# Optimization experiments

Hardware: AMD Instinct MI355X
Metric: run time of the kernel (lower is better)

## Reference

```python
import jax, jax.numpy as jnp
import numpy as np

NF = 64            # n_filter
CFAC = 3           # SinSobel c_factor: identity + sobel-x + sobel-y
FIN = NF * CFAC    # dyna block input channels (192)
FH = NF * 2        # dyna hidden (128)
FOUT = NF          # dyna output (64)
LAT = 512
N_CALLS = 6        # ceil(log2(128) - log2(2))
P_SIZES = [FH * FIN, FH, FH * FH, FH, FOUT * FH, FOUT, FOUT * FIN, FOUT]
P_TOTAL = sum(P_SIZES)  # 61824
_OFFS = np.cumsum([0] + P_SIZES)

def act(t):
    return jax.nn.leaky_relu(t, 0.2)

def conv1x1(x, w, b):
    # x [B,I,H,W], w [O,I] -> [B,O,H,W]
    return jnp.einsum('bihw,oi->bohw', x, w) + b[None, :, None, None]

def res_block(x, w0, b0, w1, b1):
    # GAN-stability style residual block with 1x1 convs
    return x + 0.1 * conv1x1(act(conv1x1(act(x), w0, b0)), w1, b1)

def depthwise3x3(x, k2d):
    C = x.shape[1]
    k = jnp.broadcast_to(k2d.astype(x.dtype), (C, 1, 3, 3))
    return jax.lax.conv_general_dilated(
        x, k, (1, 1), [(1, 1), (1, 1)],
        dimension_numbers=('NCHW', 'OIHW', 'NCHW'),
        feature_group_count=C)

SOBEL_X = jnp.array([[1., 0., -1.], [2., 0., -2.], [1., 0., -1.]], jnp.float32) / 8.0
SOBEL_Y = SOBEL_X.T
_g = jnp.exp(-0.5 * jnp.array([-1., 0., 1.], jnp.float32) ** 2)
GAUSS = jnp.outer(_g, _g)
GAUSS = GAUSS / GAUSS.sum()

def sin_sobel(x):
    return jnp.concatenate([x, depthwise3x3(x, SOBEL_X), depthwise3x3(x, SOBEL_Y)], axis=1)

def dyna_residual(x, params):
    # per-sample hypernetwork-generated 1x1-conv residual block
    B = x.shape[0]
    def take(i, shape):
        return params[:, _OFFS[i]:_OFFS[i + 1]].reshape((B,) + shape)
    w_in, b_in = take(0, (FH, FIN)), take(1, (FH,))
    w_mid, b_mid = take(2, (FH, FH)), take(3, (FH,))
    w_out, b_out = take(4, (FOUT, FH)), take(5, (FOUT,))
    w_sk, b_sk = take(6, (FOUT, FIN)), take(7, (FOUT,))
    def pconv(h, w, b):  # batched per-sample 1x1 conv
        return jnp.einsum('bihw,boi->bohw', h, w) + b[:, :, None, None]
    x_s = pconv(x, w_sk, b_sk)
    dx = pconv(x, w_in, b_in)
    dx = pconv(act(dx), w_mid, b_mid)
    dx = pconv(act(dx), w_out, b_out)
    return x_s + dx

def downsample(x):
    # GaussianSmoothing(k=3, sigma=1, pad=1) then bilinear 0.5
    # (align_corners=False bilinear at scale 0.5 == 2x2 average pooling)
    x = depthwise3x3(x, GAUSS)
    B, C, H, W = x.shape
    return x.reshape(B, C, H // 2, 2, W // 2, 2).mean(axis=(3, 5))

def lin_res(x, w1, b1, w2, b2, sw=None, sb=None):
    x_s = x if sw is None else x @ sw + sb
    return x_s + 0.1 * (act(act(x) @ w1 + b1) @ w2 + b2)

def forward(x, inj_lat, leak, in_w, in_b, inrb_w0, inrb_b0, inrb_w1, inrb_b1,
            hyp_w, hyp_b, outrb_w0, outrb_b0, outrb_w1, outrb_b1,
            l1_sw, l1_sb, l1_w1, l1_b1, l1_w2, l1_b2,
            l2_w1, l2_b1, l2_w2, l2_b2, lo_w, lo_b):
    out = conv1x1(x, in_w, in_b)
    out = res_block(out, inrb_w0, inrb_b0, inrb_w1, inrb_b1)
    leak_f = jnp.clip(leak, 0.001, 1000.0)
    dyn_params = inj_lat @ hyp_w + hyp_b  # [B, P_TOTAL], shared across calls
    out_embs = [out]
    for _ in range(N_CALLS):  # fixed small layer loop; spatial dims halve each call
        out_new = sin_sobel(out)
        out_new = dyna_residual(out_new, dyn_params)
        out = out + leak_f * out_new
        out = downsample(out)
        out_embs.append(out)
    out = res_block(out, outrb_w0, outrb_b0, outrb_w1, outrb_b1)
    h = out.mean(axis=(2, 3))  # [B, NF]
    h = lin_res(h, l1_w1, l1_b1, l1_w2, l1_b2, l1_sw, l1_sb)
    h = lin_res(h, l2_w1, l2_b1, l2_w2, l2_b2)
    lat = h @ lo_w + lo_b
    return lat, out_embs

def setup_inputs() -> dict:
    key = jax.random.key(0)
    ks = jax.random.split(key, 24)
    B, C, S = 8, 3, 128
    def rn(k, shape, scale=0.05):
        return scale * jax.random.normal(k, shape, jnp.float32)
    z = lambda n: jnp.zeros((n,), jnp.float32)
    return {
        'x': jax.random.normal(ks[0], (B, C, S, S), jnp.float32),
        'inj_lat': jax.random.normal(ks[1], (B, LAT), jnp.float32),
        'leak': jnp.array(0.1, jnp.float32),
        'in_w': rn(ks[2], (NF, C)), 'in_b': z(NF),
        'inrb_w0': rn(ks[3], (NF, NF)), 'inrb_b0': z(NF),
        'inrb_w1': rn(ks[4], (NF, NF)), 'inrb_b1': z(NF),
        'hyp_w': rn(ks[5], (LAT, P_TOTAL), 0.01), 'hyp_b': rn(ks[6], (P_TOTAL,), 0.01),
        'outrb_w0': rn(ks[7], (NF, NF)), 'outrb_b0': z(NF),
        'outrb_w1': rn(ks[8], (NF, NF)), 'outrb_b1': z(NF),
        'l1_sw': rn(ks[9], (NF, LAT)), 'l1_sb': z(LAT),
        'l1_w1': rn(ks[10], (NF, 2 * LAT)), 'l1_b1': z(2 * LAT),
        'l1_w2': rn(ks[11], (2 * LAT, LAT)), 'l1_b2': z(LAT),
        'l2_w1': rn(ks[12], (LAT, LAT)), 'l2_b1': z(LAT),
        'l2_w2': rn(ks[13], (LAT, LAT)), 'l2_b2': z(LAT),
        'lo_w': rn(ks[14], (LAT, LAT)), 'lo_b': z(LAT),
    }

def reference(x, inj_lat, leak, in_w, in_b, inrb_w0, inrb_b0, inrb_w1, inrb_b1,
              hyp_w, hyp_b, outrb_w0, outrb_b0, outrb_w1, outrb_b1,
              l1_sw, l1_sb, l1_w1, l1_b1, l1_w2, l1_b2,
              l2_w1, l2_b1, l2_w2, l2_b2, lo_w, lo_b):
    lat, out_embs = forward(x, inj_lat, leak, in_w, in_b, inrb_w0, inrb_b0, inrb_w1, inrb_b1,
                            hyp_w, hyp_b, outrb_w0, outrb_b0, outrb_w1, outrb_b1,
                            l1_sw, l1_sb, l1_w1, l1_b1, l1_w2, l1_b2,
                            l2_w1, l2_b1, l2_w2, l2_b2, lo_w, lo_b)
    return (lat, *out_embs)
```

## Files before the change

### kernel.cpp

```cpp
#include <hip/hip_runtime.h>


#define BATCH 8
#define PT 61824

typedef __attribute__((ext_vector_type(8))) short bf16x8;
typedef __attribute__((ext_vector_type(4))) float f32x4;

__device__ __forceinline__ float lrelu(float v) { return v > 0.f ? v : 0.2f * v; }

__device__ __forceinline__ short f2bf(float f) {
    union { float fv; unsigned u; } v; v.fv = f;
    return (short)((v.u + 0x7fffu + ((v.u >> 16) & 1u)) >> 16);
}

__device__ __forceinline__ unsigned cvt_pk_bf16(float lo, float hi) {
    unsigned r;
    asm("v_cvt_pk_bf16_f32 %0, %1, %2" : "=v"(r) : "v"(lo), "v"(hi));
    return r;
}
__device__ __forceinline__ short f2bf1(float f) {
    unsigned r;
    asm("v_cvt_pk_bf16_f32 %0, %1, %1" : "=v"(r) : "v"(f));
    return (short)r;
}

__global__ __launch_bounds__(256) void hyper_kernel(
    const float* __restrict__ inj, const float* __restrict__ hw,
    const float* __restrict__ hb, float* __restrict__ dyn,
    short* __restrict__ dyn16)
{
    __shared__ float s_l[512 * 8];
    __shared__ float s_part[3 * 8 * 64];
    int t = threadIdx.x;
    for (int i = t; i < 4096; i += 256) {
        int b = i >> 9, k = i & 511;
        s_l[k * 8 + b] = inj[i];
    }
    __syncthreads();
    int po = t & 63, kq = t >> 6;
    int p = blockIdx.x * 64 + po;
    float acc[8];
#pragma unroll
    for (int b = 0; b < 8; ++b) acc[b] = 0.f;
    for (int k = kq * 128; k < kq * 128 + 128; ++k) {
        float w = hw[(size_t)k * PT + p];
        float4 a0 = *(const float4*)&s_l[k * 8];
        float4 a1 = *(const float4*)&s_l[k * 8 + 4];
        acc[0] += a0.x * w; acc[1] += a0.y * w; acc[2] += a0.z * w; acc[3] += a0.w * w;
        acc[4] += a1.x * w; acc[5] += a1.y * w; acc[6] += a1.z * w; acc[7] += a1.w * w;
    }
    if (kq > 0) {
#pragma unroll
        for (int b = 0; b < 8; ++b) s_part[((kq - 1) * 8 + b) * 64 + po] = acc[b];
    }
    __syncthreads();
    if (kq == 0) {
        float bias = hb[p];
        bool isb = (p >= 24576 && p < 24704) || (p >= 41088 && p < 41216)
                || (p >= 49408 && p < 49472) || (p >= 61760);
#pragma unroll
        for (int b = 0; b < 8; ++b) {
            float v = acc[b] + s_part[b * 64 + po] + s_part[(8 + b) * 64 + po]
                    + s_part[(16 + b) * 64 + po] + bias;
            if (isb) dyn[(size_t)b * PT + p] = v;
            dyn16[(size_t)b * PT + p] = f2bf1(v);
        }
    }
}

__global__ __launch_bounds__(256) void stem_kernel(
    const float* __restrict__ x, const float* __restrict__ in_w,
    const float* __restrict__ in_b,
    const float* __restrict__ w0, const float* __restrict__ b0,
    const float* __restrict__ w1, const float* __restrict__ b1,
    float* __restrict__ out0)
{
    const int HW = 128 * 128;
    __shared__ float s_t0[64 * 68];
    __shared__ short s_vh[2 * 64 * 72];
    __shared__ float s_x[192];
    short* s_v = s_vh;
    short* s_h = s_vh + 64 * 72;
    float* s_y = (float*)s_vh;

    const int b = blockIdx.x >> 8;
    const int tile = blockIdx.x & 255;
    const int pix0 = tile * 64;
    const int t = threadIdx.x;
    const int l = t & 63, w = t >> 6;
    const int lp = l & 15, lq = l >> 4;

    if (t < 192) s_x[t] = x[(size_t)b * 3 * HW + (t >> 6) * HW + pix0 + (t & 63)];
    __syncthreads();

    for (int j = t; j < 1024; j += 256) {
        int p = j & 63, cg = j >> 6;
        float x0 = s_x[p], x1 = s_x[64 + p], x2 = s_x[128 + p];
        short pk[4];
#pragma unroll
        for (int cc = 0; cc < 4; ++cc) {
            int c = cg * 4 + cc;
            float v = in_b[c] + x0 * in_w[c * 3] + x1 * in_w[c * 3 + 1]
                    + x2 * in_w[c * 3 + 2];
            s_t0[c * 68 + p] = v;
            pk[cc] = f2bf1(lrelu(v));
        }
        *(short4*)&s_v[p * 72 + cg * 4] = make_short4(pk[0], pk[1], pk[2], pk[3]);
    }
    __syncthreads();

    const int o = w * 16 + lp;
    const f32x4 z4 = {0.f, 0.f, 0.f, 0.f};

    bf16x8 wb0[2], wb1[2];
#pragma unroll
    for (int k = 0; k < 2; ++k) {
        bf16x8 p0, p1;
#pragma unroll
        for (int e = 0; e < 8; ++e) {
            p0[e] = f2bf1(w0[o * 64 + k * 32 + lq * 8 + e]);
            p1[e] = f2bf1(w1[o * 64 + k * 32 + lq * 8 + e]);
        }
        wb0[k] = p0; wb1[k] = p1;
    }

    {
        float bi = b0[o];
        f32x4 acc[4];
#pragma unroll
        for (int mt = 0; mt < 4; ++mt) acc[mt] = z4;
#pragma unroll
        for (int k = 0; k < 2; ++k)
#pragma unroll
            for (int mt = 0; mt < 4; ++mt) {
                bf16x8 a = *(const bf16x8*)&s_v[(mt * 16 + lp) * 72 + k * 32 + lq * 8];
                acc[mt] = __builtin_amdgcn_mfma_f32_16x16x32_bf16(a, wb0[k], acc[mt], 0, 0, 0);
            }
#pragma unroll
        for (int mt = 0; mt < 4; ++mt)
#pragma unroll
            for (int r = 0; r < 4; ++r)
                s_h[(mt * 16 + lq * 4 + r) * 72 + o] = f2bf1(lrelu(acc[mt][r] + bi));
    }
    __syncthreads();

    {
        float bi = b1[o];
        f32x4 acc[4];
#pragma unroll
        for (int mt = 0; mt < 4; ++mt) acc[mt] = z4;
#pragma unroll
        for (int k = 0; k < 2; ++k)
#pragma unroll
            for (int mt = 0; mt < 4; ++mt) {
                bf16x8 a = *(const bf16x8*)&s_h[(mt * 16 + lp) * 72 + k * 32 + lq * 8];
                acc[mt] = __builtin_amdgcn_mfma_f32_16x16x32_bf16(a, wb1[k], acc[mt], 0, 0, 0);
            }
        __syncthreads();
#pragma unroll
        for (int mt = 0; mt < 4; ++mt) {
            f32x4 dv;
#pragma unroll
            for (int r = 0; r < 4; ++r) dv[r] = 0.1f * (acc[mt][r] + bi);
            *(f32x4*)&s_y[o * 68 + mt * 16 + lq * 4] = dv;
        }
    }
    __syncthreads();

#pragma unroll
    for (int v = 0; v < 4; ++v) {
        int idx = v * 1024 + t * 4;
        int oo = idx >> 6, px = idx & 63;
        f32x4 t0v = *(const f32x4*)&s_t0[oo * 68 + px];
        f32x4 dv = *(const f32x4*)&s_y[oo * 68 + px];
        f32x4 ov = t0v + dv;
        *(f32x4*)&out0[((size_t)b * 64 + oo) * HW + pix0 + px] = ov;
    }
}

template<int MT>
__global__ __launch_bounds__(256, 4) void iter_kernel(
    const float* __restrict__ cur, const float* __restrict__ dynf,
    const short* __restrict__ dynb, const float* __restrict__ leak_p,
    float* __restrict__ y, int S, int sh)
{
    constexpr int PX = MT * 16;
    constexpr int SY = (MT == 4) ? 68 : 20;
    __shared__ short s_s[PX * 192];
    __shared__ short s_h[PX * 128];
    float* s_y = (float*)s_s;

    const int HW = S * S;
    const int tilesPer = HW / PX;
    const int nwg = BATCH * tilesPer;
    const int rb = (int)blockIdx.x;
    const int lb = (rb & 7) * (nwg >> 3) + (rb >> 3);
    const int b = lb / tilesPer;
    const int tile = lb - b * tilesPer;
    const int pix0 = tile * PX;
    const int t = threadIdx.x;
    const int l = t & 63, w = t >> 6;
    const int lp = l & 15, lq = l >> 4;
    const float* base = cur + (size_t)b * 64 * HW;
    const float lk = fminf(fmaxf(leak_p[0], 0.001f), 1000.f);

    {
        const int p = (MT == 4) ? (lp + 16 * w) : lp;
        const int rxw = (p & 7) << 2;
        const int gpx = pix0 + p;
        const int row = gpx >> sh;
        const int x = gpx & (S - 1);
        const bool rm = (row > 0), rp = (row < S - 1);
        const bool le = (lp == 0) && (x > 0);
        const bool re = (lp == 15) && (x < S - 1);
        constexpr int iters = (MT == 4) ? 8 : 2;
        int* s32 = (int*)s_s;
#pragma unroll
        for (int i = 0; i < iters; ++i) {
            const int cp = (MT == 4) ? (lq + 4 * i) : (lq + 4 * w + 16 * i);
            float v0s[2], sxs[2], sys[2];
#pragma unroll
            for (int cc = 0; cc < 2; ++cc) {
                const int c = 2 * cp + cc;
                const float* ch = base + (size_t)c * HW + row * S;
                float vm = rm ? ch[x - S] : 0.f;
                float v0 = ch[x];
                float vp = rp ? ch[x + S] : 0.f;
                float elm = 0.f, el0 = 0.f, elp = 0.f, erm = 0.f, er0 = 0.f, erp = 0.f;
                if (le) { elm = rm ? ch[x - 1 - S] : 0.f; el0 = ch[x - 1]; elp = rp ? ch[x - 1 + S] : 0.f; }
                if (re) { erm = rm ? ch[x + 1 - S] : 0.f; er0 = ch[x + 1]; erp = rp ? ch[x + 1 + S] : 0.f; }
                float Lm = __shfl(vm, l - 1), L0 = __shfl(v0, l - 1), Lp = __shfl(vp, l - 1);
                float Rm = __shfl(vm, l + 1), R0 = __shfl(v0, l + 1), Rp = __shfl(vp, l + 1);
                if (lp == 0)  { Lm = elm; L0 = el0; Lp = elp; }
                if (lp == 15) { Rm = erm; R0 = er0; Rp = erp; }
                if (x == 0)     { Lm = 0.f; L0 = 0.f; Lp = 0.f; }
                if (x == S - 1) { Rm = 0.f; R0 = 0.f; Rp = 0.f; }
                v0s[cc] = v0;
                sxs[cc] = (Lm - Rm + 2.f * (L0 - R0) + Lp - Rp) * 0.125f;
                sys[cc] = (Lm + 2.f * vm + Rm - Lp - 2.f * vp - Rp) * 0.125f;
            }
            const int cpx_ = cp ^ rxw;
            s32[p * 96 + cpx_] = (int)cvt_pk_bf16(v0s[0], v0s[1]);
            s32[p * 96 + 32 + cpx_] = (int)cvt_pk_bf16(sxs[0], sxs[1]);
            s32[p * 96 + 64 + cpx_] = (int)cvt_pk_bf16(sys[0], sys[1]);
        }
    }
    __syncthreads();

    const short* wb = dynb + (size_t)b * PT;
    const float* pf = dynf + (size_t)b * PT;
    const f32x4 z4 = {0.f, 0.f, 0.f, 0.f};
    const int sx4 = (lp & 7) << 4;
    const char* ss_b = (const char*)s_s;
    const char* sh_cb = (const char*)s_h;
    char* sh_b = (char*)s_h;

    f32x4 acc_sk[MT];
#pragma unroll
    for (int mt = 0; mt < MT; ++mt) acc_sk[mt] = z4;

    {
        const float bi0 = pf[24576 + (w * 2) * 16 + lp];
        const float bi1 = pf[24576 + (w * 2 + 1) * 16 + lp];
        f32x4 acc[2][MT];
#pragma unroll
        for (int n = 0; n < 2; ++n)
#pragma unroll
            for (int mt = 0; mt < MT; ++mt) acc[n][mt] = z4;
        const int osk = w * 16 + lp;
#pragma unroll 2
        for (int k = 0; k < 6; ++k) {
            bf16x8 a[MT];
#pragma unroll
            for (int mt = 0; mt < MT; ++mt)
                a[mt] = *(const bf16x8*)(ss_b + (mt * 16 + lp) * 384 + ((k * 64 + lq * 16) ^ sx4));
#pragma unroll
            for (int n = 0; n < 2; ++n) {
                int o = (w * 2 + n) * 16 + lp;
                bf16x8 bb = *(const bf16x8*)&wb[o * 192 + k * 32 + lq * 8];
#pragma unroll
                for (int mt = 0; mt < MT; ++mt)
                    acc[n][mt] = __builtin_amdgcn_mfma_f32_16x16x32_bf16(a[mt], bb, acc[n][mt], 0, 0, 0);
            }
            {
                bf16x8 bsk = *(const bf16x8*)&wb[49472 + osk * 192 + k * 32 + lq * 8];
#pragma unroll
                for (int mt = 0; mt < MT; ++mt)
                    acc_sk[mt] = __builtin_amdgcn_mfma_f32_16x16x32_bf16(a[mt], bsk, acc_sk[mt], 0, 0, 0);
            }
        }
#pragma unroll
        for (int n = 0; n < 2; ++n) {
            int o = (w * 2 + n) * 16 + lp;
            float bi = n ? bi1 : bi0;
#pragma unroll
            for (int mt = 0; mt < MT; ++mt)
#pragma unroll
                for (int r = 0; r < 4; ++r) {
                    int row = mt * 16 + lq * 4 + r;
                    *(short*)(sh_b + row * 256 + ((o * 2) ^ ((row & 7) << 4))) =
                        f2bf1(lrelu(acc[n][mt][r] + bi));
                }
        }
    }
    __syncthreads();

    {
        const float bi0 = pf[41088 + (w * 2) * 16 + lp];
        const float bi1 = pf[41088 + (w * 2 + 1) * 16 + lp];
        f32x4 acc[2][MT];
#pragma unroll
        for (int n = 0; n < 2; ++n)
#pragma unroll
            for (int mt = 0; mt < MT; ++mt) acc[n][mt] = z4;
#pragma unroll 2
        for (int k = 0; k < 4; ++k) {
            bf16x8 a[MT];
#pragma unroll
            for (int mt = 0; mt < MT; ++mt)
                a[mt] = *(const bf16x8*)(sh_cb + (mt * 16 + lp) * 256 + ((k * 64 + lq * 16) ^ sx4));
#pragma unroll
            for (int n = 0; n < 2; ++n) {
                int o = (w * 2 + n) * 16 + lp;
                bf16x8 bb = *(const bf16x8*)&wb[24704 + o * 128 + k * 32 + lq * 8];
#pragma unroll
                for (int mt = 0; mt < MT; ++mt)
                    acc[n][mt] = __builtin_amdgcn_mfma_f32_16x16x32_bf16(a[mt], bb, acc[n][mt], 0, 0, 0);
            }
        }
        __syncthreads();
#pragma unroll
        for (int n = 0; n < 2; ++n) {
            int o = (w * 2 + n) * 16 + lp;
            float bi = n ? bi1 : bi0;
#pragma unroll
            for (int mt = 0; mt < MT; ++mt)
#pragma unroll
                for (int r = 0; r < 4; ++r) {
                    int row = mt * 16 + lq * 4 + r;
                    *(short*)(sh_b + row * 256 + ((o * 2) ^ ((row & 7) << 4))) =
                        f2bf1(lrelu(acc[n][mt][r] + bi));
                }
        }
    }
    __syncthreads();

    {
        int o = w * 16 + lp;
        const float bi = pf[49408 + o] + pf[61760 + o];
        f32x4 acc[MT];
#pragma unroll
        for (int mt = 0; mt < MT; ++mt) acc[mt] = acc_sk[mt];
#pragma unroll 2
        for (int k = 0; k < 4; ++k) {
            bf16x8 bb = *(const bf16x8*)&wb[41216 + o * 128 + k * 32 + lq * 8];
#pragma unroll
            for (int mt = 0; mt < MT; ++mt) {
                bf16x8 a = *(const bf16x8*)(sh_cb + (mt * 16 + lp) * 256 + ((k * 64 + lq * 16) ^ sx4));
                acc[mt] = __builtin_amdgcn_mfma_f32_16x16x32_bf16(a, bb, acc[mt], 0, 0, 0);
            }
        }
#pragma unroll
        for (int mt = 0; mt < MT; ++mt) {
            f32x4 dv;
#pragma unroll
            for (int r = 0; r < 4; ++r) dv[r] = acc[mt][r] + bi;
            *(f32x4*)&s_y[o * SY + mt * 16 + lq * 4] = dv;
        }
    }
    __syncthreads();

    {
        if (MT == 4) {
#pragma unroll
            for (int v = 0; v < 4; ++v) {
                int idx = v * 1024 + t * 4;
                int o = idx >> 6, px = idx & 63;
                f32x4 sv = *(const f32x4*)&s_y[o * SY + px];
                const float* cb = cur + ((size_t)b * 64 + o) * HW + pix0 + px;
                float* yb = y + ((size_t)b * 64 + o) * HW + pix0 + px;
                f32x4 cv = *(const f32x4*)cb;
                *(f32x4*)yb = cv + lk * sv;
            }
        } else {
            int o = t >> 2, px = (t & 3) * 4;
            f32x4 sv = *(const f32x4*)&s_y[o * SY + px];
            const float* cb = cur + ((size_t)b * 64 + o) * HW + pix0 + px;
            float* yb = y + ((size_t)b * 64 + o) * HW + pix0 + px;
            f32x4 cv = *(const f32x4*)cb;
            *(f32x4*)yb = cv + lk * sv;
        }
    }
}

__global__ __launch_bounds__(256) void down_kernel(
    const float* __restrict__ yin, float* __restrict__ outp,
    int S, int S2, int TW, int CPB, int tiles)
{
    __shared__ float s_in[3072];
    __shared__ float s_hb[1152];

    const float ga = 0.60653065971263342f;
    const float gs = 1.f / ((1.f + 2.f * ga) * (1.f + 2.f * ga));
    const float u0 = ga, u1 = 1.f + ga;

    const int t = threadIdx.x;
    const int nwg = (int)gridDim.x;
    const int rb = (int)blockIdx.x;
    const int bi = (rb & 7) * (nwg >> 3) + (rb >> 3);
    const int tix = bi % tiles;
    const int rem = bi / tiles;
    const int tiy = rem % tiles;
    const int cg = rem / tiles;
    const int bc0 = cg * CPB;

    const int IH = 2 * TW + 2;
    const int IW = IH;
    const int IWP = IW + 2;
    const int HS = TW + 1;
    const int gy0 = tiy * 2 * TW - 1;
    const int gx0 = tix * 2 * TW - 1;

    const int loadTot = CPB * IH * IW;
    for (int j = t; j < loadTot; j += 256) {
        int c = j / (IH * IW);
        int r = j - c * (IH * IW);
        int iy = r / IW, ix = r - iy * IW;
        int gy = gy0 + iy, gx = gx0 + ix;
        float v = 0.f;
        if (gy >= 0 && gy < S && gx >= 0 && gx < S)
            v = yin[(size_t)(bc0 + c) * S * S + gy * S + gx];
        s_in[(c * IH + iy) * IWP + ix] = v;
    }
    __syncthreads();

    const int hTot = CPB * IH * TW;
    for (int j = t; j < hTot; j += 256) {
        int c = j / (IH * TW);
        int r = j - c * (IH * TW);
        int iy = r / TW, ox = r - iy * TW;
        const float* pin = &s_in[(c * IH + iy) * IWP + 2 * ox];
        s_hb[(c * IH + iy) * HS + ox] =
            u0 * (pin[0] + pin[3]) + u1 * (pin[1] + pin[2]);
    }
    __syncthreads();

    {
        int ox = t % TW;
        int r = t / TW;
        int oy = r % TW;
        int c = r / TW;
        const float* ph = &s_hb[(c * IH + 2 * oy) * HS + ox];
        float acc = u0 * (ph[0] + ph[3 * HS]) + u1 * (ph[HS] + ph[2 * HS]);
        outp[(size_t)(bc0 + c) * S2 * S2 + (tiy * TW + oy) * S2 + tix * TW + ox] =
            acc * 0.25f * gs;
    }
}

__global__ __launch_bounds__(256) void head_a_kernel(
    const float* __restrict__ emb6,
    const float* __restrict__ w0, const float* __restrict__ b0,
    const float* __restrict__ w1, const float* __restrict__ b1,
    float* __restrict__ h)
{
    __shared__ float sm_t[256], sm_v[256], sm_r[256];
    int b = blockIdx.x, t = threadIdx.x;
    sm_t[t] = emb6[b * 256 + t];
    __syncthreads();
    {
        int o = t & 63, p = t >> 6;
        float acc = 0.f;
        for (int k = 0; k < 64; ++k) acc += w0[o * 64 + k] * lrelu(sm_t[k * 4 + p]);
        sm_v[o * 4 + p] = lrelu(acc + b0[o]);
    }
    __syncthreads();
    {
        int o = t & 63, p = t >> 6;
        float acc = 0.f;
        for (int k = 0; k < 64; ++k) acc += w1[o * 64 + k] * sm_v[k * 4 + p];
        sm_r[o * 4 + p] = sm_t[o * 4 + p] + 0.1f * (acc + b1[o]);
    }
    __syncthreads();
    if (t < 64)
        h[b * 64 + t] = 0.25f * (sm_r[t * 4] + sm_r[t * 4 + 1] + sm_r[t * 4 + 2] + sm_r[t * 4 + 3]);
}

__global__ __launch_bounds__(256) void head_b_kernel(
    const float* __restrict__ h, const float* __restrict__ w,
    const float* __restrict__ bias, float* __restrict__ t1)
{
    __shared__ float s_h[64];
    int id = blockIdx.x * 256 + threadIdx.x;
    int b = id >> 10, o = id & 1023;
    if (threadIdx.x < 64) s_h[threadIdx.x] = lrelu(h[b * 64 + threadIdx.x]);
    __syncthreads();
    float acc = 0.f;
    for (int k = 0; k < 64; ++k) acc += s_h[k] * w[k * 1024 + o];
    t1[b * 1024 + o] = lrelu(acc + bias[o]);
}

__global__ __launch_bounds__(256) void head_c_kernel(
    const float* __restrict__ h, const float* __restrict__ t1,
    const float* __restrict__ sw, const float* __restrict__ sb,
    const float* __restrict__ w2, const float* __restrict__ b2,
    float* __restrict__ h1)
{
    __shared__ float s_t[8 * 128];
    __shared__ float s_h[8 * 64];
    int oblk = blockIdx.x & 1, chunk = blockIdx.x >> 1;
    int t = threadIdx.x;
    int o = oblk * 256 + t;
    for (int j = t; j < 1024; j += 256) {
        int b = j >> 7, kk = j & 127;
        s_t[j] = t1[b * 1024 + chunk * 128 + kk];
    }
    if (chunk == 0)
        for (int j = t; j < 512; j += 256) s_h[j] = h[j];
    __syncthreads();
    float acc[8];
#pragma unroll
    for (int b = 0; b < 8; ++b) acc[b] = 0.f;
    for (int kk = 0; kk < 128; ++kk) {
        float wv = w2[(chunk * 128 + kk) * 512 + o];
#pragma unroll
        for (int b = 0; b < 8; ++b) acc[b] += s_t[b * 128 + kk] * wv;
    }
#pragma unroll
    for (int b = 0; b < 8; ++b) acc[b] *= 0.1f;
    if (chunk == 0) {
        for (int k = 0; k < 64; ++k) {
            float wv = sw[k * 512 + o];
#pragma unroll
            for (int b = 0; b < 8; ++b) acc[b] += s_h[b * 64 + k] * wv;
        }
        float c0 = sb[o] + 0.1f * b2[o];
#pragma unroll
        for (int b = 0; b < 8; ++b) acc[b] += c0;
    }
#pragma unroll
    for (int b = 0; b < 8; ++b) atomicAdd(&h1[b * 512 + o], acc[b]);
}

__global__ __launch_bounds__(256) void head_d_kernel(
    const float* __restrict__ h1, const float* __restrict__ w,
    const float* __restrict__ bias, float* __restrict__ z3)
{
    __shared__ float s_u[8 * 64];
    int oblk = blockIdx.x & 1, chunk = blockIdx.x >> 1;
    int t = threadIdx.x;
    int o = oblk * 256 + t;
    for (int j = t; j < 512; j += 256) {
        int b = j >> 6, kk = j & 63;
        s_u[j] = lrelu(h1[b * 512 + chunk * 64 + kk]);
    }
    __syncthreads();
    float acc[8];
#pragma unroll
    for (int b = 0; b < 8; ++b) acc[b] = 0.f;
    for (int kk = 0; kk < 64; ++kk) {
        float wv = w[(chunk * 64 + kk) * 512 + o];
#pragma unroll
        for (int b = 0; b < 8; ++b) acc[b] += s_u[b * 64 + kk] * wv;
    }
    if (chunk == 0) {
        float c0 = bias[o];
#pragma unroll
        for (int b = 0; b < 8; ++b) acc[b] += c0;
    }
#pragma unroll
    for (int b = 0; b < 8; ++b) atomicAdd(&z3[b * 512 + o], acc[b]);
}

__global__ __launch_bounds__(256) void head_e_kernel(
    const float* __restrict__ h1, const float* __restrict__ z3,
    const float* __restrict__ w, const float* __restrict__ bias,
    float* __restrict__ h2)
{
    __shared__ float s_u[8 * 64];
    int oblk = blockIdx.x & 1, chunk = blockIdx.x >> 1;
    int t = threadIdx.x;
    int o = oblk * 256 + t;
    for (int j = t; j < 512; j += 256) {
        int b = j >> 6, kk = j & 63;
        s_u[j] = lrelu(z3[b * 512 + chunk * 64 + kk]);
    }
    __syncthreads();
    float acc[8];
#pragma unroll
    for (int b = 0; b < 8; ++b) acc[b] = 0.f;
    for (int kk = 0; kk < 64; ++kk) {
        float wv = w[(chunk * 64 + kk) * 512 + o];
#pragma unroll
        for (int b = 0; b < 8; ++b) acc[b] += s_u[b * 64 + kk] * wv;
    }
#pragma unroll
    for (int b = 0; b < 8; ++b) acc[b] *= 0.1f;
    if (chunk == 0) {
        float c0 = 0.1f * bias[o];
#pragma unroll
        for (int b = 0; b < 8; ++b) acc[b] += h1[b * 512 + o] + c0;
    }
#pragma unroll
    for (int b = 0; b < 8; ++b) atomicAdd(&h2[b * 512 + o], acc[b]);
}

__global__ __launch_bounds__(256) void head_f_kernel(
    const float* __restrict__ h2, const float* __restrict__ w,
    const float* __restrict__ bias, float* __restrict__ lat)
{
    __shared__ float s_u[8 * 64];
    int oblk = blockIdx.x & 1, chunk = blockIdx.x >> 1;
    int t = threadIdx.x;
    int o = oblk * 256 + t;
    for (int j = t; j < 512; j += 256) {
        int b = j >> 6, kk = j & 63;
        s_u[j] = h2[b * 512 + chunk * 64 + kk];
    }
    __syncthreads();
    float acc[8];
#pragma unroll
    for (int b = 0; b < 8; ++b) acc[b] = 0.f;
    for (int kk = 0; kk < 64; ++kk) {
        float wv = w[(chunk * 64 + kk) * 512 + o];
#pragma unroll
        for (int b = 0; b < 8; ++b) acc[b] += s_u[b * 64 + kk] * wv;
    }
    if (chunk == 0) {
        float c0 = bias[o];
#pragma unroll
        for (int b = 0; b < 8; ++b) acc[b] += c0;
    }
#pragma unroll
    for (int b = 0; b < 8; ++b) atomicAdd(&lat[b * 512 + o], acc[b]);
}

extern "C" void kernel_launch(void* const* d_in, const int* in_sizes, int n_in,
                              void* d_out, int out_size, void* d_ws, size_t ws_size,
                              hipStream_t stream) {
    const float* x      = (const float*)d_in[0];
    const float* inj    = (const float*)d_in[1];
    const float* leak   = (const float*)d_in[2];
    const float* in_w   = (const float*)d_in[3];
    const float* in_b   = (const float*)d_in[4];
    const float* inrb_w0 = (const float*)d_in[5];
    const float* inrb_b0 = (const float*)d_in[6];
    const float* inrb_w1 = (const float*)d_in[7];
    const float* inrb_b1 = (const float*)d_in[8];
    const float* hyp_w  = (const float*)d_in[9];
    const float* hyp_b  = (const float*)d_in[10];
    const float* outrb_w0 = (const float*)d_in[11];
    const float* outrb_b0 = (const float*)d_in[12];
    const float* outrb_w1 = (const float*)d_in[13];
    const float* outrb_b1 = (const float*)d_in[14];
    const float* l1_sw  = (const float*)d_in[15];
    const float* l1_sb  = (const float*)d_in[16];
    const float* l1_w1  = (const float*)d_in[17];
    const float* l1_b1  = (const float*)d_in[18];
    const float* l1_w2  = (const float*)d_in[19];
    const float* l1_b2  = (const float*)d_in[20];
    const float* l2_w1  = (const float*)d_in[21];
    const float* l2_b1  = (const float*)d_in[22];
    const float* l2_w2  = (const float*)d_in[23];
    const float* l2_b2  = (const float*)d_in[24];
    const float* lo_w   = (const float*)d_in[25];
    const float* lo_b   = (const float*)d_in[26];

    float* out = (float*)d_out;
    float* dyn = (float*)d_ws;
    float* ybuf = dyn + (size_t)BATCH * PT;
    short* dyn16 = (short*)(ybuf + (size_t)BATCH * 64 * 16384);
    float* hbuf = (float*)(dyn16 + (size_t)BATCH * PT);
    float* t1buf = hbuf + 512;
    float* h1buf = t1buf + 8192;
    float* z3buf = h1buf + 4096;
    float* h2buf = z3buf + 4096;

    hipMemsetAsync(h1buf, 0, (4096 * 3) * sizeof(float), stream);
    hipMemsetAsync(out, 0, 4096 * sizeof(float), stream);

    hyper_kernel<<<PT / 64, 256, 0, stream>>>(inj, hyp_w, hyp_b, dyn, dyn16);

    size_t cur = 4096;
    stem_kernel<<<BATCH * 256, 256, 0, stream>>>(
        x, in_w, in_b, inrb_w0, inrb_b0, inrb_w1, inrb_b1, out + cur);

    int S = 128, sh = 7;
    for (int i = 0; i < 6; ++i) {
        if (S >= 64) {
            iter_kernel<4><<<BATCH * (S * S / 64), 256, 0, stream>>>(
                out + cur, dyn, dyn16, leak, ybuf, S, sh);
        } else {
            iter_kernel<1><<<BATCH * (S * S / 16), 256, 0, stream>>>(
                out + cur, dyn, dyn16, leak, ybuf, S, sh);
        }
        int S2 = S >> 1;
        size_t nxt = cur + (size_t)BATCH * 64 * S * S;
        int TW = (S2 >= 16) ? 16 : S2;
        int tiles = S2 / TW;
        int CPB = 256 / (TW * TW);
        if (CPB < 1) CPB = 1;
        int grid = (BATCH * 64 / CPB) * tiles * tiles;
        down_kernel<<<grid, 256, 0, stream>>>(ybuf, out + nxt, S, S2, TW, CPB, tiles);
        cur = nxt;
        S = S2; sh -= 1;
    }

    head_a_kernel<<<BATCH, 256, 0, stream>>>(
        out + cur, outrb_w0, outrb_b0, outrb_w1, outrb_b1, hbuf);
    head_b_kernel<<<32, 256, 0, stream>>>(hbuf, l1_w1, l1_b1, t1buf);
    head_c_kernel<<<16, 256, 0, stream>>>(hbuf, t1buf, l1_sw, l1_sb, l1_w2, l1_b2, h1buf);
    head_d_kernel<<<16, 256, 0, stream>>>(h1buf, l2_w1, l2_b1, z3buf);
    head_e_kernel<<<16, 256, 0, stream>>>(h1buf, z3buf, l2_w2, l2_b2, h2buf);
    head_f_kernel<<<16, 256, 0, stream>>>(h2buf, lo_w, lo_b, out);
}
```

Baseline: 507.5 us.

## Restructure sobel perception with separable column sums and shared-memory halo exchange

For the 4-tile configuration, each thread now loads all 16 channel columns at once and computes separable vertical sums (smooth and difference). Horizontal neighbours come from lane shuffles, and the edge lanes between waves exchange values through a small halo buffer in shared memory, so the per-lane edge loads and redundant 3x3 arithmetic go away. It also raises wave priority around the MFMA loop of the first dynamic conv. The cost is higher register pressure from the 48 buffered floats and an extra barrier.

```diff
diff --git a/kernel.cpp b/kernel.cpp
--- a/kernel.cpp
+++ b/kernel.cpp
@@ -205,8 +205,90 @@
     const float* base = cur + (size_t)b * 64 * HW;
     const float lk = fminf(fmaxf(leak_p[0], 0.001f), 1000.f);
 
-    {
-        const int p = (MT == 4) ? (lp + 16 * w) : lp;
+    if constexpr (MT == 4) {
+        const int p = lp + 16 * w;
+        const int rxw = (p & 7) << 2;
+        const int gpx = pix0 + p;
+        const int row = gpx >> sh;
+        const int x = gpx & (S - 1);
+        const bool rm = (row > 0), rp = (row < S - 1);
+        float* halo_a = (float*)s_h;
+        float* halo_d = halo_a + 640;
+        int* s32 = (int*)s_s;
+
+        float vm[16], vv[16], vp[16];
+        const float* col = base + row * S + x;
+#pragma unroll
+        for (int j = 0; j < 16; ++j) {
+            const int c = 2 * (lq + 4 * (j >> 1)) + (j & 1);
+            const float* ch = col + (size_t)c * HW;
+            vm[j] = rm ? ch[-S] : 0.f;
+            vv[j] = ch[0];
+            vp[j] = rp ? ch[S] : 0.f;
+        }
+        float a[16], d[16];
+#pragma unroll
+        for (int j = 0; j < 16; ++j) {
+            a[j] = vm[j] + 2.f * vv[j] + vp[j];
+            d[j] = vm[j] - vp[j];
+        }
+        if (w == 0 || w == 3) {
+            const bool left = (w == 0) && (lp == 0);
+            const bool right = (w == 3) && (lp == 15);
+            if (left || right) {
+                const int xe = left ? x - 1 : x + 1;
+                const int slot = left ? 8 : 9;
+                const bool valid = (xe >= 0) && (xe < S);
+                const float* ecol = base + row * S + xe;
+#pragma unroll
+                for (int j = 0; j < 16; ++j) {
+                    const int c = 2 * (lq + 4 * (j >> 1)) + (j & 1);
+                    float em = 0.f, e0 = 0.f, ep = 0.f;
+                    if (valid) {
+                        const float* ch = ecol + (size_t)c * HW;
+                        em = rm ? ch[-S] : 0.f;
+                        e0 = ch[0];
+                        ep = rp ? ch[S] : 0.f;
+                    }
+                    halo_a[slot * 64 + c] = em + 2.f * e0 + ep;
+                    halo_d[slot * 64 + c] = em - ep;
+                }
+            }
+        }
+        if (lp == 0 || lp == 15) {
+            const int slot = 2 * w + (lp == 15 ? 1 : 0);
+#pragma unroll
+            for (int j = 0; j < 16; ++j) {
+                const int c = 2 * (lq + 4 * (j >> 1)) + (j & 1);
+                halo_a[slot * 64 + c] = a[j];
+                halo_d[slot * 64 + c] = d[j];
+            }
+        }
+        __syncthreads();
+        const int slotL = (w == 0) ? 8 : 2 * (w - 1) + 1;
+        const int slotR = (w == 3) ? 9 : 2 * (w + 1);
+#pragma unroll
+        for (int i = 0; i < 8; ++i) {
+            float sx2[2], sy2[2];
+#pragma unroll
+            for (int cc = 0; cc < 2; ++cc) {
+                const int j = 2 * i + cc;
+                const int c = 2 * (lq + 4 * i) + cc;
+                float aL = __shfl(a[j], l - 1), dL = __shfl(d[j], l - 1);
+                float aR = __shfl(a[j], l + 1), dR = __shfl(d[j], l + 1);
+                if (lp == 0)  { aL = halo_a[slotL * 64 + c]; dL = halo_d[slotL * 64 + c]; }
+                if (lp == 15) { aR = halo_a[slotR * 64 + c]; dR = halo_d[slotR * 64 + c]; }
+                sx2[cc] = (aL - aR) * 0.125f;
+                sy2[cc] = (dL + 2.f * d[j] + dR) * 0.125f;
+            }
+            const int cp = lq + 4 * i;
+            const int cpx_ = cp ^ rxw;
+            s32[p * 96 + cpx_] = (int)cvt_pk_bf16(vv[2 * i], vv[2 * i + 1]);
+            s32[p * 96 + 32 + cpx_] = (int)cvt_pk_bf16(sx2[0], sx2[1]);
+            s32[p * 96 + 64 + cpx_] = (int)cvt_pk_bf16(sy2[0], sy2[1]);
+        }
+    } else {
+        const int p = lp;
         const int rxw = (p & 7) << 2;
         const int gpx = pix0 + p;
         const int row = gpx >> sh;
@@ -214,11 +296,10 @@
         const bool rm = (row > 0), rp = (row < S - 1);
         const bool le = (lp == 0) && (x > 0);
         const bool re = (lp == 15) && (x < S - 1);
-        constexpr int iters = (MT == 4) ? 8 : 2;
         int* s32 = (int*)s_s;
 #pragma unroll
-        for (int i = 0; i < iters; ++i) {
-            const int cp = (MT == 4) ? (lq + 4 * i) : (lq + 4 * w + 16 * i);
+        for (int i = 0; i < 2; ++i) {
+            const int cp = lq + 4 * w + 16 * i;
             float v0s[2], sxs[2], sys[2];
 #pragma unroll
             for (int cc = 0; cc < 2; ++cc) {
@@ -269,6 +350,7 @@
 #pragma unroll
             for (int mt = 0; mt < MT; ++mt) acc[n][mt] = z4;
         const int osk = w * 16 + lp;
+        __builtin_amdgcn_s_setprio(1);
 #pragma unroll 2
         for (int k = 0; k < 6; ++k) {
             bf16x8 a[MT];
@@ -290,6 +372,7 @@
                     acc_sk[mt] = __builtin_amdgcn_mfma_f32_16x16x32_bf16(a[mt], bsk, acc_sk[mt], 0, 0, 0);
             }
         }
+        __builtin_amdgcn_s_setprio(0);
 #pragma unroll
         for (int n = 0; n < 2; ++n) {
             int o = (w * 2 + n) * 16 + lp;
```

Measured after the change: 505.9 us. About the same (-0.3%).
